# Performance work log

Hardware: AMD Instinct MI355X
Metric: run time of the kernel (lower is better)

Reference implementation:

```python
import jax, jax.numpy as jnp
import numpy as np

# ---- static part graph (matches torch.nonzero row-major edge order) ----
ADJ = np.array([[0,1,0,0,0,0],
                [1,0,1,1,1,1],
                [0,1,0,0,0,0],
                [0,1,0,0,0,0],
                [0,1,0,0,0,1],
                [0,1,0,0,1,0]], dtype=np.int64)
EDGES = [(int(u), int(v)) for u, v in np.argwhere(ADJ)]  # 12 edges
P = ADJ.shape[0]                 # 6 part nodes (cls_p - 1)
PART_LIST = [[] for _ in range(P)]
for u, v in EDGES:
    PART_LIST[v].append(u)
DEG = [len(l) for l in PART_LIST]  # [1,5,1,1,2,2], sum = 12
CLS_P = P + 1
IN_DIM, HID = 256, 10
N, H, W = 4, 64, 64


def spatial_coords(h, w):
    """[8,h,w] coord features, same as generate_spatial_batch (vectorized)."""
    ws = np.arange(w, dtype=np.float32); hs = np.arange(h, dtype=np.float32)
    xmin = ws / w * 2 - 1; xmax = (ws + 1) / w * 2 - 1; xctr = (xmin + xmax) / 2
    ymin = hs / h * 2 - 1; ymax = (hs + 1) / h * 2 - 1; yctr = (ymin + ymax) / 2
    f = np.zeros((h, w, 8), np.float32)
    f[..., 0] = xmin[None, :]; f[..., 1] = ymin[:, None]
    f[..., 2] = xmax[None, :]; f[..., 3] = ymax[:, None]
    f[..., 4] = xctr[None, :]; f[..., 5] = yctr[:, None]
    f[..., 6] = 1.0 / w;       f[..., 7] = 1.0 / h
    return jnp.asarray(f.transpose(2, 0, 1))


def conv1x1(x, w, b=None):
    y = jnp.einsum('nchw,oc->nohw', x, w)
    return y if b is None else y + b[None, :, None, None]


def conv3x3(x, w):
    return jax.lax.conv_general_dilated(x, w, (1, 1), 'SAME',
                                        dimension_numbers=('NCHW', 'OIHW', 'NCHW'))


def bn(x, g, b, eps=1e-5):
    mu = x.mean((0, 2, 3), keepdims=True)
    var = ((x - mu) ** 2).mean((0, 2, 3), keepdims=True)
    return (x - mu) * jax.lax.rsqrt(var + eps) * g[None, :, None, None] + b[None, :, None, None]


def setup_inputs() -> dict:
    key = jax.random.key(0)
    ks = jax.random.split(key, 16)
    s = 0.05
    return {
        'xp':      jax.random.normal(ks[0], (N, IN_DIM, H, W), jnp.float32),
        'p_nodes': jax.random.normal(ks[1], (CLS_P, N, HID, H, W), jnp.float32),
        'p_atts':  jax.random.normal(ks[2], (CLS_P, N, 1, H, W), jnp.float32),
        'W_key':  jax.random.normal(ks[3], (64, IN_DIM + 8), jnp.float32) * s,
        'b_key':  jnp.zeros((64,), jnp.float32),
        'W_q':    jax.random.normal(ks[4], (64, IN_DIM + 8), jnp.float32) * s,
        'b_q':    jnp.zeros((64,), jnp.float32),
        'W_att':  jax.random.normal(ks[5], (sum(DEG), IN_DIM + 1), jnp.float32) * s,
        'b_att':  jnp.zeros((sum(DEG),), jnp.float32),
        'W_proj': jax.random.normal(ks[6], (HID, IN_DIM), jnp.float32) * s,
        'g_proj': jnp.ones((HID,), jnp.float32),
        'bt_proj': jnp.zeros((HID,), jnp.float32),
        'W_rel1': jax.random.normal(ks[7], (2 * HID, 2 * HID, 3, 3), jnp.float32) * s,
        'g_rel1': jnp.ones((2 * HID,), jnp.float32),
        'bt_rel1': jnp.zeros((2 * HID,), jnp.float32),
        'W_rel2': jax.random.normal(ks[8], (HID, 2 * HID), jnp.float32) * s,
        'b_rel2': jnp.zeros((HID,), jnp.float32),
        'Wg':    jax.random.normal(ks[9], (P, 2, 2 * HID), jnp.float32) * s,
        'bg':    jnp.zeros((P, 2), jnp.float32),
        'Wc':    jax.random.normal(ks[10], (P, HID, 2 * HID), jnp.float32) * s,
        'g_can': jnp.ones((P, HID), jnp.float32),
        'bt_can': jnp.zeros((P, HID), jnp.float32),
    }


def reference(xp, p_nodes, p_atts,
              W_key, b_key, W_q, b_q, W_att, b_att,
              W_proj, g_proj, bt_proj, W_rel1, g_rel1, bt_rel1, W_rel2, b_rel2,
              Wg, bg, Wc, g_can, bt_can):
    n, c, h, w = xp.shape
    L = h * w
    coord = jnp.broadcast_to(spatial_coords(h, w), (n, 8, h, w))

    # ---- Dep_Context (vectorized over the P part nodes) ----
    feat = jnp.concatenate([xp, coord], axis=1)                 # [n, 264, h, w]
    key_f = conv1x1(feat, W_key, b_key).reshape(n, 64, L)       # [n, 64, L]
    p_att = p_atts[1:]                                          # [P, n, 1, h, w]
    norm = jax.nn.softmax(p_att.reshape(P, n, L), axis=-1)      # [P, n, L]
    hu_c = jnp.einsum('ncl,pnl->pnc', xp.reshape(n, c, L), norm)       # [P, n, 256]
    co_c = jnp.einsum('ncl,pnl->pnc', coord.reshape(n, 8, L), norm)    # [P, n, 8]
    cen = jnp.concatenate([hu_c, co_c], axis=-1)                # [P, n, 264]
    q = jnp.einsum('pnf,of->pno', cen, W_q) + b_q               # [P, n, 64]
    energy = jnp.einsum('pno,nol->pnl', q, key_f)               # [P, n, L]
    attn = jax.nn.sigmoid(energy).reshape(P, n, 1, h, w)
    one_m = 1.0 - p_att
    F_dep_att = attn * one_m                                    # [P, n, 1, h, w]
    F_dep = attn * xp[None] * one_m                             # [P, n, 256, h, w]

    # ---- Contexture attention heads (per-node conv, deg_i output channels) ----
    att_logits, att_soft = [], []
    off = 0
    for i in range(P):
        d = DEG[i]
        inp = jnp.concatenate([F_dep_att[i], xp], axis=1)       # [n, 257, h, w]
        logit = conv1x1(inp, W_att[off:off + d], b_att[off:off + d])
        att_logits.append(logit)
        att_soft.append(jax.nn.softmax(logit, axis=1))
        off += d

    # ---- Dependency messages per edge ----
    def dependency(hv, hu_ctx, dep_att):
        msg = jax.nn.relu(bn(conv1x1(hu_ctx * dep_att, W_proj), g_proj, bt_proj))
        x = jnp.concatenate([msg, hv], axis=1)                  # [n, 20, h, w]
        x = jax.nn.relu(bn(conv3x3(x, W_rel1), g_rel1, bt_rel1))
        return jax.nn.sigmoid(conv1x1(x, W_rel2, b_rel2))       # [n, 10, h, w]

    msgs = [None] * P
    for u, v in EDGES:
        ch = PART_LIST[u].index(v)
        # NB: original code indexes p_node_list with the raw edge target v
        m = dependency(p_nodes[v], F_dep[u], att_soft[u][:, ch:ch + 1])
        msgs[v] = m if msgs[v] is None else msgs[v] + m

    # ---- ConvGRU node updates ----
    new_nodes = [p_nodes[0]]
    for i in range(P):
        h_cur, msg = p_nodes[i + 1], msgs[i]
        gates = conv1x1(jnp.concatenate([msg, h_cur], axis=1), Wg[i], bg[i])
        r = jax.nn.sigmoid(gates[:, 0:1]); z = jax.nn.sigmoid(gates[:, 1:2])
        cnm = conv1x1(jnp.concatenate([msg, r * h_cur], axis=1), Wc[i])
        cnm = jax.nn.leaky_relu(bn(cnm, g_can[i], bt_can[i]), 0.01)  # InPlaceABNSync default
        new_nodes.append((1.0 - z) * h_cur + z * cnm)

    xp_new = jnp.stack(new_nodes)                               # [cls_p, n, 10, h, w]
    fdep_att = jnp.concatenate(att_logits, axis=1)              # [n, 12, h, w]
    return xp_new, fdep_att
```

## Files before the change

kernel.cpp:

```cpp
#include <hip/hip_runtime.h>
#include <math.h>

#define L 4096

__constant__ int c_EV[12]   = {1,0,2,3,4,5,1,1,1,5,1,4};
__constant__ int c_INOFF[7] = {0,1,6,7,8,10,12};
__constant__ int c_INE[12]  = {1, 0,6,7,8,10, 2, 3, 4,11, 5,9};

__device__ inline float sigmf(float x){ return 1.f/(1.f+expf(-x)); }

__global__ __launch_bounds__(256) void k_softmax_norm(const float* __restrict__ p_atts,
                                                      float* __restrict__ norm){
  int pn = blockIdx.x;
  const float* src = p_atts + (size_t)(pn + 4) * L;
  float* dst = norm + (size_t)pn * L;
  __shared__ float red[256];
  int tid = threadIdx.x;
  float m = -1e30f;
  for (int l = tid; l < L; l += 256) m = fmaxf(m, src[l]);
  red[tid] = m; __syncthreads();
  for (int s = 128; s; s >>= 1){ if (tid < s) red[tid] = fmaxf(red[tid], red[tid+s]); __syncthreads(); }
  m = red[0]; __syncthreads();
  float sum = 0.f;
  for (int l = tid; l < L; l += 256) sum += expf(src[l] - m);
  red[tid] = sum; __syncthreads();
  for (int s = 128; s; s >>= 1){ if (tid < s) red[tid] += red[tid+s]; __syncthreads(); }
  float inv = 1.f / red[0];
  for (int l = tid; l < L; l += 256) dst[l] = expf(src[l] - m) * inv;
}

__device__ inline float coord_feat(int cc, int l){
  int h = l >> 6, w = l & 63;
  const float s = 2.f / 64.f;
  switch (cc){
    case 0: return w * s - 1.f;
    case 1: return h * s - 1.f;
    case 2: return (w + 1) * s - 1.f;
    case 3: return (h + 1) * s - 1.f;
    case 4: return (w + 0.5f) * s - 1.f;
    case 5: return (h + 0.5f) * s - 1.f;
    default: return 1.f / 64.f;
  }
}

__global__ __launch_bounds__(256) void k_centroid(const float* __restrict__ xp,
                                                  const float* __restrict__ norm,
                                                  float* __restrict__ cen){
  int c = blockIdx.x;
  int n = blockIdx.y;
  int tid = threadIdx.x;
  float acc[6];
#pragma unroll
  for (int p = 0; p < 6; p++) acc[p] = 0.f;
  const float* nr0 = norm + (size_t)n * L;
  if (c < 256){
    const float* xr = xp + ((size_t)n * 256 + c) * L;
    for (int l = tid; l < L; l += 256){
      float xv = xr[l];
#pragma unroll
      for (int p = 0; p < 6; p++) acc[p] = fmaf(xv, nr0[(size_t)p * 4 * L + l], acc[p]);
    }
  } else {
    int cc = c - 256;
    for (int l = tid; l < L; l += 256){
      float xv = coord_feat(cc, l);
#pragma unroll
      for (int p = 0; p < 6; p++) acc[p] = fmaf(xv, nr0[(size_t)p * 4 * L + l], acc[p]);
    }
  }
#pragma unroll
  for (int p = 0; p < 6; p++){
    for (int off = 32; off; off >>= 1) acc[p] += __shfl_xor(acc[p], off, 64);
  }
  __shared__ float red[6][4];
  int wv = tid >> 6;
  if ((tid & 63) == 0){
#pragma unroll
    for (int p = 0; p < 6; p++) red[p][wv] = acc[p];
  }
  __syncthreads();
  if (tid < 6){
    float s = red[tid][0] + red[tid][1] + red[tid][2] + red[tid][3];
    cen[(size_t)(tid * 4 + n) * 264 + c] = s;
  }
}

__global__ __launch_bounds__(256) void k_qk(const float* __restrict__ cen,
                                            const float* __restrict__ W_q, const float* __restrict__ b_q,
                                            const float* __restrict__ W_key, const float* __restrict__ b_key,
                                            float* __restrict__ qk, float* __restrict__ qb){
  int pn = blockIdx.x;
  int tid = threadIdx.x;
  __shared__ float cen_s[264];
  __shared__ float qs[64];
  __shared__ float part[256];
  for (int i = tid; i < 264; i += 256) cen_s[i] = cen[(size_t)pn * 264 + i];
  __syncthreads();
  int o = tid >> 2, pr = tid & 3;
  {
    float a = 0.f;
    int f0 = pr * 66;
    for (int j = 0; j < 66; j++){ int f = f0 + j; a = fmaf(cen_s[f], W_q[o * 264 + f], a); }
    part[tid] = a;
  }
  __syncthreads();
  if (pr == 0) qs[o] = part[tid] + part[tid + 1] + part[tid + 2] + part[tid + 3] + b_q[o];
  __syncthreads();
  for (int c = tid; c < 264; c += 256){
    float a = 0.f;
    for (int oo = 0; oo < 64; oo++) a = fmaf(qs[oo], W_key[oo * 264 + c], a);
    qk[(size_t)pn * 264 + c] = a;
  }
  if (tid < 64) part[tid] = qs[tid] * b_key[tid];
  __syncthreads();
  if (tid == 0){
    float a = 0.f;
    for (int oo = 0; oo < 64; oo++) a += part[oo];
    qb[pn] = a;
  }
}

__global__ __launch_bounds__(256) void k_wt(const float* __restrict__ W_rel1, float* __restrict__ wt2){
  for (int i = threadIdx.x; i < 3600; i += 256){
    int co = i % 10; int t = i / 10;
    int k = t % 9; t /= 9;
    int h = t & 1; int ci = t >> 1;
    wt2[i] = W_rel1[(((h * 10 + co) * 20) + ci) * 9 + k];
  }
}

__global__ __launch_bounds__(256) void k_pixel(const float* __restrict__ xp,
                                              const float* __restrict__ p_atts,
                                              const float* __restrict__ W_att, const float* __restrict__ b_att,
                                              const float* __restrict__ W_proj,
                                              const float* __restrict__ qk, const float* __restrict__ qb,
                                              float* __restrict__ out_fdep,
                                              float* __restrict__ s_edge,
                                              float* __restrict__ proj_x){
  __shared__ float s_watt[256 * 12];
  __shared__ float s_wproj[256 * 12];
  __shared__ float s_qk[256 * 8];
  __shared__ float s_qkt[48];
  __shared__ float pacc[4][28][64];
  __shared__ float w0[12], ba[12], qbs[6];
  int n = blockIdx.y;
  int tid = threadIdx.x;
  int wv = tid >> 6, w = tid & 63;
  int l = blockIdx.x * 64 + w;
  for (int i = tid; i < 256 * 12; i += 256){ int c = i / 12, j = i % 12; s_watt[i] = W_att[j * 257 + 1 + c]; }
  for (int i = tid; i < 256 * 12; i += 256){ int c = i / 12, k = i % 12; s_wproj[i] = (k < 10) ? W_proj[k * 256 + c] : 0.f; }
  for (int i = tid; i < 256 * 8; i += 256){ int c = i >> 3, p = i & 7; s_qk[i] = (p < 6) ? qk[((size_t)(p * 4 + n)) * 264 + c] : 0.f; }
  if (tid < 48){ int p = tid >> 3, cc = tid & 7; s_qkt[tid] = qk[((size_t)(p * 4 + n)) * 264 + 256 + cc]; }
  if (tid < 12){ w0[tid] = W_att[tid * 257]; ba[tid] = b_att[tid]; }
  if (tid < 6) qbs[tid] = qb[tid * 4 + n];
  __syncthreads();

  float a[32];
#pragma unroll
  for (int f = 0; f < 32; f++) a[f] = 0.f;
  const float* xpn = xp + (size_t)n * 256 * L + l;
  int c0 = wv * 64;
#pragma unroll 2
  for (int cc = 0; cc < 64; cc++){
    int c = c0 + cc;
    float xv = xpn[(size_t)c * L];
    float4 wa0 = *(const float4*)(s_watt + c * 12);
    float4 wa1 = *(const float4*)(s_watt + c * 12 + 4);
    float4 wa2 = *(const float4*)(s_watt + c * 12 + 8);
    float4 wp0 = *(const float4*)(s_wproj + c * 12);
    float4 wp1 = *(const float4*)(s_wproj + c * 12 + 4);
    float4 wp2 = *(const float4*)(s_wproj + c * 12 + 8);
    float4 wq0 = *(const float4*)(s_qk + c * 8);
    float4 wq1 = *(const float4*)(s_qk + c * 8 + 4);
    a[0]  = fmaf(xv, wa0.x, a[0]);  a[1]  = fmaf(xv, wa0.y, a[1]);
    a[2]  = fmaf(xv, wa0.z, a[2]);  a[3]  = fmaf(xv, wa0.w, a[3]);
    a[4]  = fmaf(xv, wa1.x, a[4]);  a[5]  = fmaf(xv, wa1.y, a[5]);
    a[6]  = fmaf(xv, wa1.z, a[6]);  a[7]  = fmaf(xv, wa1.w, a[7]);
    a[8]  = fmaf(xv, wa2.x, a[8]);  a[9]  = fmaf(xv, wa2.y, a[9]);
    a[10] = fmaf(xv, wa2.z, a[10]); a[11] = fmaf(xv, wa2.w, a[11]);
    a[12] = fmaf(xv, wp0.x, a[12]); a[13] = fmaf(xv, wp0.y, a[13]);
    a[14] = fmaf(xv, wp0.z, a[14]); a[15] = fmaf(xv, wp0.w, a[15]);
    a[16] = fmaf(xv, wp1.x, a[16]); a[17] = fmaf(xv, wp1.y, a[17]);
    a[18] = fmaf(xv, wp1.z, a[18]); a[19] = fmaf(xv, wp1.w, a[19]);
    a[20] = fmaf(xv, wp2.x, a[20]); a[21] = fmaf(xv, wp2.y, a[21]);
    a[24] = fmaf(xv, wq0.x, a[24]); a[25] = fmaf(xv, wq0.y, a[25]);
    a[26] = fmaf(xv, wq0.z, a[26]); a[27] = fmaf(xv, wq0.w, a[27]);
    a[28] = fmaf(xv, wq1.x, a[28]); a[29] = fmaf(xv, wq1.y, a[29]);
  }
#pragma unroll
  for (int f = 0; f < 12; f++) pacc[wv][f][w] = a[f];
#pragma unroll
  for (int k = 0; k < 10; k++) pacc[wv][12 + k][w] = a[12 + k];
#pragma unroll
  for (int p = 0; p < 6; p++) pacc[wv][22 + p][w] = a[24 + p];
  __syncthreads();
  for (int idx = tid; idx < 28 * 64; idx += 256){
    int f = idx >> 6, ww = idx & 63;
    pacc[0][f][ww] = pacc[0][f][ww] + pacc[1][f][ww] + pacc[2][f][ww] + pacc[3][f][ww];
  }
  __syncthreads();
  if (tid < 64){
    float accA[12], accP[10], accE[6];
#pragma unroll
    for (int j = 0; j < 12; j++) accA[j] = pacc[0][j][w];
#pragma unroll
    for (int k = 0; k < 10; k++) accP[k] = pacc[0][12 + k][w];
#pragma unroll
    for (int p = 0; p < 6; p++) accE[p] = pacc[0][22 + p][w];

    float cf[8];
    { int hh = l >> 6, ww2 = l & 63; const float s = 2.f / 64.f;
      cf[0] = ww2 * s - 1.f; cf[1] = hh * s - 1.f; cf[2] = (ww2 + 1) * s - 1.f; cf[3] = (hh + 1) * s - 1.f;
      cf[4] = (ww2 + 0.5f) * s - 1.f; cf[5] = (hh + 0.5f) * s - 1.f; cf[6] = 1.f / 64.f; cf[7] = 1.f / 64.f; }
    float sat[6];
#pragma unroll
    for (int p = 0; p < 6; p++){
      float e = accE[p] + qbs[p];
#pragma unroll
      for (int cc = 0; cc < 8; cc++) e = fmaf(cf[cc], s_qkt[p * 8 + cc], e);
      float aa = sigmf(e);
      float pa = p_atts[((size_t)(p + 1) * 4 + n) * L + l];
      sat[p] = aa * (1.f - pa);
    }
    const int part_of[12] = {0,1,1,1,1,1,2,3,4,4,5,5};
    float lg[12];
#pragma unroll
    for (int j = 0; j < 12; j++){
      lg[j] = accA[j] + w0[j] * sat[part_of[j]] + ba[j];
      out_fdep[((size_t)n * 12 + j) * L + l] = lg[j];
    }
    const int gs[6] = {0,1,6,7,8,10}, gd[6] = {1,5,1,1,2,2};
    float sm[12];
#pragma unroll
    for (int g = 0; g < 6; g++){
      int s0 = gs[g], d = gd[g];
      float mx = lg[s0];
      for (int t = 1; t < d; t++) mx = fmaxf(mx, lg[s0 + t]);
      float ssum = 0.f;
      for (int t = 0; t < d; t++){ float e2 = expf(lg[s0 + t] - mx); sm[s0 + t] = e2; ssum += e2; }
      float inv = 1.f / ssum;
      for (int t = 0; t < d; t++) sm[s0 + t] *= inv;
    }
#pragma unroll
    for (int e = 0; e < 12; e++) s_edge[((size_t)e * 4 + n) * L + l] = sat[part_of[e]] * sm[e];
#pragma unroll
    for (int k = 0; k < 10; k++) proj_x[((size_t)n * 10 + k) * L + l] = accP[k];
  }
}

__global__ __launch_bounds__(256) void k_msg_stats(const float* __restrict__ proj_x,
                                                   const float* __restrict__ s_edge,
                                                   float* __restrict__ mu, float* __restrict__ istd){
  int e = blockIdx.x / 10, k = blockIdx.x % 10;
  int tid = threadIdx.x;
  float s1 = 0.f, s2 = 0.f;
  for (int idx = tid; idx < 4 * L; idx += 256){
    int n = idx >> 12, l = idx & (L - 1);
    float t = proj_x[((size_t)n * 10 + k) * L + l] * s_edge[((size_t)e * 4 + n) * L + l];
    s1 += t; s2 += t * t;
  }
  __shared__ float r1[256], r2[256];
  r1[tid] = s1; r2[tid] = s2; __syncthreads();
  for (int s = 128; s; s >>= 1){ if (tid < s){ r1[tid] += r1[tid+s]; r2[tid] += r2[tid+s]; } __syncthreads(); }
  if (tid == 0){
    float m = r1[0] / 16384.f, v = r2[0] / 16384.f - m * m;
    mu[blockIdx.x] = m; istd[blockIdx.x] = rsqrtf(v + 1e-5f);
  }
}

__global__ __launch_bounds__(256) void k_conv3(const float* __restrict__ proj_x,
                                               const float* __restrict__ s_edge,
                                               const float* __restrict__ mu, const float* __restrict__ istd,
                                               const float* __restrict__ g_proj, const float* __restrict__ bt_proj,
                                               const float* __restrict__ p_nodes,
                                               const float* __restrict__ wt2,
                                               float* __restrict__ y,
                                               float* __restrict__ ypart){
  __shared__ float xs[20][6][66];
  __shared__ float scs[10], sbs[10];
  __shared__ float red[4][20];
  int rb = blockIdx.x, n = blockIdx.y;
  int e = blockIdx.z >> 1, h = blockIdx.z & 1;
  int v = c_EV[e];
  int tid = threadIdx.x;
  if (tid < 10){
    int ek = e * 10 + tid;
    float s = istd[ek] * g_proj[tid];
    scs[tid] = s; sbs[tid] = bt_proj[tid] - mu[ek] * s;
  }
  __syncthreads();
  for (int i = tid; i < 20 * 6 * 66; i += 256){
    int col = i % 66; int rr = (i / 66) % 6; int ch = i / 396;
    int grow = rb * 4 - 1 + rr; int gcol = col - 1;
    float vv = 0.f;
    if (grow >= 0 && grow < 64 && gcol >= 0 && gcol < 64){
      int pix = grow * 64 + gcol;
      if (ch < 10){
        float t = proj_x[((size_t)n * 10 + ch) * L + pix] * s_edge[((size_t)e * 4 + n) * L + pix];
        vv = fmaxf(t * scs[ch] + sbs[ch], 0.f);
      } else {
        vv = p_nodes[(((size_t)v * 4 + n) * 10 + (ch - 10)) * L + pix];
      }
    }
    xs[ch][rr][col] = vv;
  }
  __syncthreads();
  int r = tid >> 6, w = tid & 63;
  float acc[10];
#pragma unroll
  for (int co = 0; co < 10; co++) acc[co] = 0.f;
  for (int ci = 0; ci < 20; ci++){
    float x[3][3];
#pragma unroll
    for (int ky = 0; ky < 3; ky++)
#pragma unroll
      for (int kx = 0; kx < 3; kx++) x[ky][kx] = xs[ci][r + ky][w + kx];
    const float* wp = wt2 + (ci * 2 + h) * 90;
#pragma unroll
    for (int ky = 0; ky < 3; ky++)
#pragma unroll
      for (int kx = 0; kx < 3; kx++){
#pragma unroll
        for (int co = 0; co < 10; co++)
          acc[co] = fmaf(x[ky][kx], wp[(ky * 3 + kx) * 10 + co], acc[co]);
      }
  }
  int row = rb * 4 + r;
  int ch0 = h * 10;
#pragma unroll
  for (int co = 0; co < 10; co++)
    y[(((size_t)e * 4 + n) * 20 + ch0 + co) * L + row * 64 + w] = acc[co];
#pragma unroll
  for (int co = 0; co < 10; co++){
    float s1 = acc[co];
    float s2 = acc[co] * acc[co];
    for (int off = 32; off; off >>= 1){ s1 += __shfl_xor(s1, off, 64); s2 += __shfl_xor(s2, off, 64); }
    if (w == 0){ red[r][2 * co] = s1; red[r][2 * co + 1] = s2; }
  }
  __syncthreads();
  if (tid < 20){
    int co = tid >> 1, which = tid & 1;
    float s = red[0][tid] + red[1][tid] + red[2][tid] + red[3][tid];
    ypart[(((size_t)(e * 20 + ch0 + co) * 64) + n * 16 + rb) * 2 + which] = s;
  }
}

__global__ __launch_bounds__(64) void k_red(const float* __restrict__ part,
                                            float* __restrict__ mu, float* __restrict__ istd){
  int ent = blockIdx.x;
  int t = threadIdx.x;
  const float* p = part + ((size_t)ent * 64 + t) * 2;
  float s1 = p[0], s2 = p[1];
  for (int off = 32; off; off >>= 1){ s1 += __shfl_xor(s1, off, 64); s2 += __shfl_xor(s2, off, 64); }
  if (t == 0){
    float m = s1 / 16384.f, v = s2 / 16384.f - m * m;
    mu[ent] = m; istd[ent] = rsqrtf(v + 1e-5f);
  }
}

__global__ __launch_bounds__(256) void k_mout_gru(const float* __restrict__ y,
                                                  const float* __restrict__ mu_y, const float* __restrict__ istd_y,
                                                  const float* __restrict__ g_rel1, const float* __restrict__ bt_rel1,
                                                  const float* __restrict__ W_rel2, const float* __restrict__ b_rel2,
                                                  const float* __restrict__ p_nodes,
                                                  const float* __restrict__ Wg, const float* __restrict__ bg,
                                                  const float* __restrict__ Wc,
                                                  float* __restrict__ cnm, float* __restrict__ zbuf,
                                                  float* __restrict__ cpart){
  int i = blockIdx.z, n = blockIdx.y;
  int tid = threadIdx.x;
  int l = blockIdx.x * 256 + tid;
  __shared__ float w2[200], wc[200], wg[40], bgs[2];
  __shared__ float sc[5][20], sb[5][20];
  __shared__ float red[4][20];
  int ne = c_INOFF[i + 1] - c_INOFF[i];
  for (int t = tid; t < 200; t += 256){ w2[t] = W_rel2[t]; wc[t] = Wc[i * 200 + t]; }
  if (tid < 40) wg[tid] = Wg[i * 40 + tid];
  if (tid < 2) bgs[tid] = bg[i * 2 + tid];
  if (tid < ne * 20){
    int ei = tid / 20, c = tid % 20;
    int e = c_INE[c_INOFF[i] + ei];
    int ec = e * 20 + c;
    float s = istd_y[ec] * g_rel1[c];
    sc[ei][c] = s; sb[ei][c] = bt_rel1[c] - mu_y[ec] * s;
  }
  __syncthreads();
  float m[10];
#pragma unroll
  for (int k = 0; k < 10; k++) m[k] = 0.f;
  for (int ei = 0; ei < ne; ei++){
    int e = c_INE[c_INOFF[i] + ei];
    float z[20];
#pragma unroll
    for (int c = 0; c < 20; c++){
      float t = y[(((size_t)e * 4 + n) * 20 + c) * L + l];
      z[c] = fmaxf(t * sc[ei][c] + sb[ei][c], 0.f);
    }
#pragma unroll
    for (int k = 0; k < 10; k++){
      float a = b_rel2[k];
#pragma unroll
      for (int c = 0; c < 20; c++) a = fmaf(w2[k * 20 + c], z[c], a);
      m[k] += sigmf(a);
    }
  }
  float h[10];
#pragma unroll
  for (int k = 0; k < 10; k++) h[k] = p_nodes[(((size_t)(i + 1) * 4 + n) * 10 + k) * L + l];
  float g0 = bgs[0], g1 = bgs[1];
#pragma unroll
  for (int k = 0; k < 10; k++){
    g0 = fmaf(wg[k], m[k], g0); g0 = fmaf(wg[10 + k], h[k], g0);
    g1 = fmaf(wg[20 + k], m[k], g1); g1 = fmaf(wg[30 + k], h[k], g1);
  }
  float r = sigmf(g0), zz = sigmf(g1);
  zbuf[((size_t)i * 4 + n) * L + l] = zz;
  float cv[10];
#pragma unroll
  for (int k = 0; k < 10; k++){
    float a = 0.f;
#pragma unroll
    for (int c = 0; c < 10; c++){
      a = fmaf(wc[k * 20 + c], m[c], a);
      a = fmaf(wc[k * 20 + 10 + c], r * h[c], a);
    }
    cv[k] = a;
    cnm[(((size_t)i * 4 + n) * 10 + k) * L + l] = a;
  }
  int wv = tid >> 6, w = tid & 63;
#pragma unroll
  for (int k = 0; k < 10; k++){
    float s1 = cv[k], s2 = cv[k] * cv[k];
    for (int off = 32; off; off >>= 1){ s1 += __shfl_xor(s1, off, 64); s2 += __shfl_xor(s2, off, 64); }
    if (w == 0){ red[wv][2 * k] = s1; red[wv][2 * k + 1] = s2; }
  }
  __syncthreads();
  if (tid < 20){
    float s = red[0][tid] + red[1][tid] + red[2][tid] + red[3][tid];
    int k = tid >> 1, which = tid & 1;
    cpart[(((size_t)(i * 10 + k) * 64) + n * 16 + blockIdx.x) * 2 + which] = s;
  }
}

__global__ __launch_bounds__(256) void k_out(const float* __restrict__ cnm, const float* __restrict__ zbuf,
                                             const float* __restrict__ p_nodes,
                                             const float* __restrict__ mu, const float* __restrict__ istd,
                                             const float* __restrict__ g_can, const float* __restrict__ bt_can,
                                             float* __restrict__ out){
  int idx = blockIdx.x * 256 + threadIdx.x;
  const int NODE = 4 * 10 * L;
  if (idx < NODE){ out[idx] = p_nodes[idx]; return; }
  int j = idx - NODE;
  int l = j & (L - 1); int r = j >> 12;
  int k = r % 10; r /= 10; int n = r & 3; int i = r >> 2;
  int ik = i * 10 + k;
  float c = cnm[j];
  float cn = (c - mu[ik]) * istd[ik] * g_can[ik] + bt_can[ik];
  cn = cn > 0.f ? cn : 0.01f * cn;
  float z = zbuf[((size_t)i * 4 + n) * L + l];
  float h = p_nodes[idx];
  out[idx] = (1.f - z) * h + z * cn;
}

extern "C" void kernel_launch(void* const* d_in, const int* in_sizes, int n_in,
                              void* d_out, int out_size, void* d_ws, size_t ws_size,
                              hipStream_t stream){
  (void)in_sizes; (void)n_in; (void)out_size; (void)ws_size;
  const float* xp      = (const float*)d_in[0];
  const float* p_nodes = (const float*)d_in[1];
  const float* p_atts  = (const float*)d_in[2];
  const float* W_key   = (const float*)d_in[3];
  const float* b_key   = (const float*)d_in[4];
  const float* W_q     = (const float*)d_in[5];
  const float* b_q     = (const float*)d_in[6];
  const float* W_att   = (const float*)d_in[7];
  const float* b_att   = (const float*)d_in[8];
  const float* W_proj  = (const float*)d_in[9];
  const float* g_proj  = (const float*)d_in[10];
  const float* bt_proj = (const float*)d_in[11];
  const float* W_rel1  = (const float*)d_in[12];
  const float* g_rel1  = (const float*)d_in[13];
  const float* bt_rel1 = (const float*)d_in[14];
  const float* W_rel2  = (const float*)d_in[15];
  const float* b_rel2  = (const float*)d_in[16];
  const float* Wg      = (const float*)d_in[17];
  const float* bg      = (const float*)d_in[18];
  const float* Wc      = (const float*)d_in[19];
  const float* g_can   = (const float*)d_in[20];
  const float* bt_can  = (const float*)d_in[21];

  float* out      = (float*)d_out;
  float* fdep_out = out + (size_t)7 * 4 * 10 * L;

  float* w = (float*)d_ws;
  size_t off = 0;
  auto alloc = [&](size_t nf){ float* p = w + off; off += nf; return p; };
  float* norm    = alloc((size_t)6 * 4 * L);
  float* cen     = alloc(6 * 4 * 264);
  float* qk      = alloc(6 * 4 * 264);
  float* qb      = alloc(24);
  float* wt2     = alloc(3600);
  float* proj_x  = alloc((size_t)4 * 10 * L);
  float* s_edge  = alloc((size_t)12 * 4 * L);
  float* mu_msg  = alloc(120);
  float* istd_msg= alloc(120);
  float* ybuf    = alloc((size_t)12 * 4 * 20 * L);
  float* ypart   = alloc(240 * 64 * 2);
  float* cpart   = alloc(60 * 64 * 2);
  float* mu_y    = alloc(240);
  float* istd_y  = alloc(240);
  float* cnm     = alloc((size_t)6 * 4 * 10 * L);
  float* zbuf    = alloc((size_t)6 * 4 * L);
  float* mu_c    = alloc(60);
  float* istd_c  = alloc(60);

  k_wt<<<1, 256, 0, stream>>>(W_rel1, wt2);
  k_softmax_norm<<<24, 256, 0, stream>>>(p_atts, norm);
  { dim3 g(264, 4); k_centroid<<<g, 256, 0, stream>>>(xp, norm, cen); }
  k_qk<<<24, 256, 0, stream>>>(cen, W_q, b_q, W_key, b_key, qk, qb);
  { dim3 g(64, 4); k_pixel<<<g, 256, 0, stream>>>(xp, p_atts, W_att, b_att, W_proj, qk, qb, fdep_out, s_edge, proj_x); }
  k_msg_stats<<<120, 256, 0, stream>>>(proj_x, s_edge, mu_msg, istd_msg);
  { dim3 g(16, 4, 24); k_conv3<<<g, 256, 0, stream>>>(proj_x, s_edge, mu_msg, istd_msg, g_proj, bt_proj, p_nodes, wt2, ybuf, ypart); }
  k_red<<<240, 64, 0, stream>>>(ypart, mu_y, istd_y);
  { dim3 g(16, 4, 6); k_mout_gru<<<g, 256, 0, stream>>>(ybuf, mu_y, istd_y, g_rel1, bt_rel1, W_rel2, b_rel2,
                                                        p_nodes, Wg, bg, Wc, cnm, zbuf, cpart); }
  k_red<<<60, 64, 0, stream>>>(cpart, mu_c, istd_c);
  k_out<<<(7 * 4 * 10 * L) / 256, 256, 0, stream>>>(cnm, zbuf, p_nodes, mu_c, istd_c, g_can, bt_can, out);
}
```

Measured before the change: 169.0 us.

## Replace LDS halo tile in conv3x3 with direct row loads and wave shuffles

The 3x3 convolution kernel no longer stages a 20x6x66 input halo tile in shared memory behind two block barriers. Each thread now loads its own pixel plus the rows above and below straight from global memory. Horizontal neighbours come from cross-lane shuffles within the 64-wide wavefront, which matches the 64-pixel image row. This removes LDS traffic, the staging loop's index arithmetic and the barriers. In exchange, each input row is fetched up to three times through the cache, and every thread recomputes the BN scale and shift from global memory.

```diff
diff --git a/kernel.cpp b/kernel.cpp
--- a/kernel.cpp
+++ b/kernel.cpp
@@ -276,66 +276,86 @@
                                                const float* __restrict__ wt2,
                                                float* __restrict__ y,
                                                float* __restrict__ ypart){
-  __shared__ float xs[20][6][66];
-  __shared__ float scs[10], sbs[10];
   __shared__ float red[4][20];
   int rb = blockIdx.x, n = blockIdx.y;
   int e = blockIdx.z >> 1, h = blockIdx.z & 1;
   int v = c_EV[e];
   int tid = threadIdx.x;
-  if (tid < 10){
-    int ek = e * 10 + tid;
-    float s = istd[ek] * g_proj[tid];
-    scs[tid] = s; sbs[tid] = bt_proj[tid] - mu[ek] * s;
-  }
-  __syncthreads();
-  for (int i = tid; i < 20 * 6 * 66; i += 256){
-    int col = i % 66; int rr = (i / 66) % 6; int ch = i / 396;
-    int grow = rb * 4 - 1 + rr; int gcol = col - 1;
-    float vv = 0.f;
-    if (grow >= 0 && grow < 64 && gcol >= 0 && gcol < 64){
-      int pix = grow * 64 + gcol;
-      if (ch < 10){
-        float t = proj_x[((size_t)n * 10 + ch) * L + pix] * s_edge[((size_t)e * 4 + n) * L + pix];
-        vv = fmaxf(t * scs[ch] + sbs[ch], 0.f);
-      } else {
-        vv = p_nodes[(((size_t)v * 4 + n) * 10 + (ch - 10)) * L + pix];
-      }
-    }
-    xs[ch][rr][col] = vv;
-  }
-  __syncthreads();
-  int r = tid >> 6, w = tid & 63;
+  int wv = tid >> 6, w = tid & 63;
+  int row = rb * 4 + wv;
+  float mLm = (w == 0) ? 0.f : 1.f;
+  float mRm = (w == 63) ? 0.f : 1.f;
+
+  float scs[10], sbs[10];
+#pragma unroll
+  for (int k = 0; k < 10; k++){
+    int ek = e * 10 + k;
+    float s = istd[ek] * g_proj[k];
+    scs[k] = s; sbs[k] = bt_proj[k] - mu[ek] * s;
+  }
+  const size_t enL = ((size_t)e * 4 + n) * L;
+  const float* se = s_edge + enL;
+
   float acc[10];
 #pragma unroll
   for (int co = 0; co < 10; co++) acc[co] = 0.f;
-  for (int ci = 0; ci < 20; ci++){
-    float x[3][3];
-#pragma unroll
-    for (int ky = 0; ky < 3; ky++)
-#pragma unroll
-      for (int kx = 0; kx < 3; kx++) x[ky][kx] = xs[ci][r + ky][w + kx];
+
+#pragma unroll 2
+  for (int ci = 0; ci < 10; ci++){
+    const float* pr = proj_x + ((size_t)n * 10 + ci) * L;
+    float a = 0.f, b, c = 0.f;
+    { int pix = row * 64 + w; float t = pr[pix] * se[pix]; b = fmaxf(fmaf(t, scs[ci], sbs[ci]), 0.f); }
+    if (row > 0){ int pix = (row - 1) * 64 + w; float t = pr[pix] * se[pix]; a = fmaxf(fmaf(t, scs[ci], sbs[ci]), 0.f); }
+    if (row < 63){ int pix = (row + 1) * 64 + w; float t = pr[pix] * se[pix]; c = fmaxf(fmaf(t, scs[ci], sbs[ci]), 0.f); }
+    float aL = __shfl_up(a, 1) * mLm;
+    float aR = __shfl_down(a, 1) * mRm;
+    float bL = __shfl_up(b, 1) * mLm;
+    float bR = __shfl_down(b, 1) * mRm;
+    float cL = __shfl_up(c, 1) * mLm;
+    float cR = __shfl_down(c, 1) * mRm;
     const float* wp = wt2 + (ci * 2 + h) * 90;
 #pragma unroll
-    for (int ky = 0; ky < 3; ky++)
-#pragma unroll
-      for (int kx = 0; kx < 3; kx++){
-#pragma unroll
-        for (int co = 0; co < 10; co++)
-          acc[co] = fmaf(x[ky][kx], wp[(ky * 3 + kx) * 10 + co], acc[co]);
-      }
-  }
-  int row = rb * 4 + r;
+    for (int co = 0; co < 10; co++){
+      float s0 = fmaf(aL, wp[co], fmaf(a, wp[10 + co], aR * wp[20 + co]));
+      s0 = fmaf(bL, wp[30 + co], fmaf(b, wp[40 + co], fmaf(bR, wp[50 + co], s0)));
+      s0 = fmaf(cL, wp[60 + co], fmaf(c, wp[70 + co], fmaf(cR, wp[80 + co], s0)));
+      acc[co] += s0;
+    }
+  }
+#pragma unroll 2
+  for (int ci = 10; ci < 20; ci++){
+    const float* pn = p_nodes + (((size_t)v * 4 + n) * 10 + (ci - 10)) * L;
+    float a = 0.f, b, c = 0.f;
+    b = pn[row * 64 + w];
+    if (row > 0)  a = pn[(row - 1) * 64 + w];
+    if (row < 63) c = pn[(row + 1) * 64 + w];
+    float aL = __shfl_up(a, 1) * mLm;
+    float aR = __shfl_down(a, 1) * mRm;
+    float bL = __shfl_up(b, 1) * mLm;
+    float bR = __shfl_down(b, 1) * mRm;
+    float cL = __shfl_up(c, 1) * mLm;
+    float cR = __shfl_down(c, 1) * mRm;
+    const float* wp = wt2 + (ci * 2 + h) * 90;
+#pragma unroll
+    for (int co = 0; co < 10; co++){
+      float s0 = fmaf(aL, wp[co], fmaf(a, wp[10 + co], aR * wp[20 + co]));
+      s0 = fmaf(bL, wp[30 + co], fmaf(b, wp[40 + co], fmaf(bR, wp[50 + co], s0)));
+      s0 = fmaf(cL, wp[60 + co], fmaf(c, wp[70 + co], fmaf(cR, wp[80 + co], s0)));
+      acc[co] += s0;
+    }
+  }
+
   int ch0 = h * 10;
 #pragma unroll
   for (int co = 0; co < 10; co++)
-    y[(((size_t)e * 4 + n) * 20 + ch0 + co) * L + row * 64 + w] = acc[co];
+    y[(enL * 20) + ((size_t)(ch0 + co)) * L + row * 64 + w] = acc[co];
+
 #pragma unroll
   for (int co = 0; co < 10; co++){
     float s1 = acc[co];
     float s2 = acc[co] * acc[co];
     for (int off = 32; off; off >>= 1){ s1 += __shfl_xor(s1, off, 64); s2 += __shfl_xor(s2, off, 64); }
-    if (w == 0){ red[r][2 * co] = s1; red[r][2 * co + 1] = s2; }
+    if (w == 0){ red[wv][2 * co] = s1; red[wv][2 * co + 1] = s2; }
   }
   __syncthreads();
   if (tid < 20){
```

After: 162.8 us. -3.7%, faster.
